# Kernel tuning notes

Measured on AMD Instinct MI355X. Metric: run time of the kernel, lower is better.

## Reference

```python
import jax, jax.numpy as jnp
import numpy as np

N_NODES = 102400   # 256 graphs x 400 nodes
N_EDGES = 1638400  # avg degree 16
C_IN = 128
C_OUT = 128
N_SAGE = 3         # gnn_num
G = 256            # num graphs
M = 400            # nodes per graph (equal-sized -> to_dense_batch is a reshape)


def setup_inputs() -> dict:
    key = jax.random.key(0)
    ks = jax.random.split(key, 6)
    x = jax.random.normal(ks[0], (N_NODES, C_IN), dtype=jnp.float32)
    edge_index = jax.random.randint(ks[1], (2, N_EDGES), 0, N_NODES, dtype=jnp.int32)
    # nodes sorted by graph id, equal graph sizes (matches to_dense_batch assumptions)
    batch = (jnp.arange(N_NODES, dtype=jnp.int32) // M)
    s_in = 1.0 / np.sqrt(C_IN)
    s_out = 1.0 / np.sqrt(C_OUT)
    W_g = jax.random.normal(ks[2], (C_IN, C_OUT), dtype=jnp.float32) * s_in
    b_g = jnp.zeros((C_OUT,), dtype=jnp.float32)
    W_l = jax.random.normal(ks[3], (N_SAGE, C_OUT, C_OUT), dtype=jnp.float32) * s_out  # neighbor lin
    b_l = jnp.zeros((N_SAGE, C_OUT), dtype=jnp.float32)
    W_r = jax.random.normal(ks[4], (N_SAGE, C_OUT, C_OUT), dtype=jnp.float32) * s_out  # root lin (no bias in PyG)
    return {"x": x, "W_g": W_g, "b_g": b_g, "W_l": W_l, "b_l": b_l,
            "W_r": W_r, "edge_index": edge_index, "batch": batch}


def _gcn_conv(x, W, b, src, dst):
    # PyG GCNConv: h = x W; add self loops; norm = d^{-1/2}_src * d^{-1/2}_dst,
    # deg = in-degree at dst counting the self loop; aggregate at dst; add bias.
    h = x @ W                                                     # [N, C_out]
    ones = jnp.ones((N_EDGES,), dtype=h.dtype)
    deg = jax.ops.segment_sum(ones, dst, num_segments=N_NODES) + 1.0
    dinv = jax.lax.rsqrt(deg)                                     # [N]
    norm = dinv[src] * dinv[dst]                                  # [E]
    agg = jax.ops.segment_sum(h[src] * norm[:, None], dst, num_segments=N_NODES)
    agg = agg + h * (dinv * dinv)[:, None]                        # self-loop term
    return agg + b


def _sage_conv(x, W_l, b_l, W_r, src, dst):
    # PyG SAGEConv (mean aggr): out = mean_{j in N(i)} x_j @ W_l + b_l + x @ W_r
    ones = jnp.ones((N_EDGES,), dtype=x.dtype)
    cnt = jax.ops.segment_sum(ones, dst, num_segments=N_NODES)
    s = jax.ops.segment_sum(x[src], dst, num_segments=N_NODES)
    mean = s / jnp.maximum(cnt, 1.0)[:, None]
    return mean @ W_l + b_l + x @ W_r


def _to_dense(x):
    # equal-sized graphs with nodes sorted by batch -> to_dense_batch == reshape
    return x.reshape(G, M, C_OUT)


def reference(x, W_g, b_g, W_l, b_l, W_r, edge_index, batch):
    src, dst = edge_index[0], edge_index[1]
    x = jax.nn.relu(_gcn_conv(x, W_g, b_g, src, dst))
    outs = [_to_dense(x)]
    for i in range(N_SAGE):
        x = jax.nn.relu(_sage_conv(x, W_l[i], b_l[i], W_r[i], src, dst))
        outs.append(_to_dense(x))
    return jnp.stack(outs)  # [N_SAGE+1, G, M, C_OUT]
```

## Files before the change

kernel.cpp:

```cpp
#include <hip/hip_runtime.h>

#define C 128
#define SLOT 64
typedef __attribute__((ext_vector_type(8))) short bf16x8;
typedef __attribute__((ext_vector_type(4))) float f32x4;

__device__ __forceinline__ unsigned short f2bf_rtn(float f) {
    unsigned u = __float_as_uint(f);
    return (unsigned short)((u + 0x7fff + ((u >> 16) & 1)) >> 16);
}
__device__ __forceinline__ float bflo(unsigned u) { return __uint_as_float(u << 16); }
__device__ __forceinline__ float bfhi(unsigned u) { return __uint_as_float(u & 0xffff0000u); }

__device__ __forceinline__ void gload_lds16(const unsigned short* g, unsigned short* l) {
    __builtin_amdgcn_global_load_lds(
        (const __attribute__((address_space(1))) void*)g,
        (__attribute__((address_space(3))) void*)l, 16, 0, 0);
}


__global__ void deg_rank_kernel(const int* __restrict__ ei, int* __restrict__ deg,
                                int* __restrict__ rank, int E) {
    int e = blockIdx.x * blockDim.x + threadIdx.x;
    if (e < E) rank[e] = atomicAdd(&deg[ei[E + e]], 1);
}

__global__ void prep_kernel(const int* __restrict__ deg, float* __restrict__ dinv,
                            float* __restrict__ cinv, int n) {
    int i = blockIdx.x * blockDim.x + threadIdx.x;
    if (i < n) {
        int d = deg[i];
        dinv[i] = rsqrtf((float)(d + 1));
        cinv[i] = 1.0f / (float)max(d, 1);
    }
}


__device__ __forceinline__ void split_bf16(float w, unsigned short& hb, unsigned short& lb) {
    unsigned u = __float_as_uint(w);
    hb = (unsigned short)(u >> 16);
    float hf = __uint_as_float(u & 0xffff0000u);
    lb = (unsigned short)(__float_as_uint(w - hf) >> 16);
}

__global__ __launch_bounds__(256) void wprep_gcn(const float* __restrict__ Wg,
                                                 unsigned short* __restrict__ dst) {
    int idx = blockIdx.x * 256 + threadIdx.x;
    if (idx >= 2 * 128 * 64) return;
    int k64 = idx & 63, ch = (idx >> 6) & 127, chunk = idx >> 13;
    int k = chunk * 64 + k64;
    unsigned short hb, lb;
    split_bf16(Wg[(size_t)k * 128 + ch], hb, lb);
    int pos = (((k64 >> 3) ^ (ch & 7)) << 3) | (k64 & 7);
    size_t base = ((size_t)chunk * 2) * 8192 + ch * 64 + pos;
    dst[base] = hb;
    dst[base + 8192] = lb;
}

__global__ __launch_bounds__(256) void wprep_fused(const float* __restrict__ Wl,
        const float* __restrict__ Wr, unsigned short* __restrict__ dst) {
    int idx = blockIdx.x * 256 + threadIdx.x;
    if (idx >= 3 * 4 * 128 * 64) return;
    int k64 = idx & 63, ch = (idx >> 6) & 127, chunk = (idx >> 13) & 3, layer = idx >> 15;
    int k = chunk * 64 + k64;
    float w = (k < 128) ? Wl[((size_t)layer * 128 + k) * 128 + ch]
                        : Wr[((size_t)layer * 128 + (k - 128)) * 128 + ch];
    unsigned short hb, lb;
    split_bf16(w, hb, lb);
    int pos = (((k64 >> 3) ^ (ch & 7)) << 3) | (k64 & 7);
    size_t base = (((size_t)layer * 4 + chunk) * 2) * 8192 + ch * 64 + pos;
    dst[base] = hb;
    dst[base + 8192] = lb;
}

__global__ __launch_bounds__(256) void csr_gemm_kernel(
        const int* __restrict__ ei, const int* __restrict__ rank,
        int* __restrict__ csr, int E,
        const float* __restrict__ x, const unsigned short* __restrict__ Wp,
        const float* __restrict__ dinv, unsigned short* __restrict__ outbf) {
    __shared__ unsigned short Bs[2][128][64];
    const int b2 = blockIdx.x >> 1;
    const int t = threadIdx.x;

    if (!(blockIdx.x & 1)) {
        const int base = b2 * 1024 + t * 4;
        int4 s4 = *(const int4*)(ei + base);
        int4 d4 = *(const int4*)(ei + E + base);
        int4 r4 = *(const int4*)(rank + base);
        if (r4.x < SLOT) csr[(d4.x << 6) + r4.x] = s4.x;
        if (r4.y < SLOT) csr[(d4.y << 6) + r4.y] = s4.y;
        if (r4.z < SLOT) csr[(d4.z << 6) + r4.z] = s4.z;
        if (r4.w < SLOT) csr[(d4.w << 6) + r4.w] = s4.w;
        return;
    }

    unsigned short* BsFlat = &Bs[0][0][0];
    const int lane = t & 63;
    const int wv = t >> 6;
    const int rowbase = b2 * 64 + wv * 16;
    const int arow = rowbase + (lane & 15);
    const int kq = lane >> 4;

    f32x4 acc[8];
#pragma unroll
    for (int f = 0; f < 8; f++) acc[f] = (f32x4){0.f, 0.f, 0.f, 0.f};

#pragma unroll
    for (int c = 0; c < 2; c++) {
        __syncthreads();
        {
            const unsigned short* srcW = Wp + (size_t)c * 16384;
#pragma unroll
            for (int i = 0; i < 8; i++)
                gload_lds16(srcW + (wv * 8 + i) * 512 + lane * 8,
                            BsFlat + (wv * 8 + i) * 512);
        }
        bf16x8 Ah[2], Al[2];
#pragma unroll
        for (int j = 0; j < 2; j++) {
            const float* base = x + (size_t)arow * C + c * 64 + j * 32;
            float4 x0 = ((const float4*)base)[kq * 2];
            float4 x1 = ((const float4*)base)[kq * 2 + 1];
            float xv[8] = {x0.x, x0.y, x0.z, x0.w, x1.x, x1.y, x1.z, x1.w};
#pragma unroll
            for (int q = 0; q < 8; q++) {
                unsigned u = __float_as_uint(xv[q]);
                Ah[j][q] = (short)(u >> 16);
                float hf = __uint_as_float(u & 0xffff0000u);
                Al[j][q] = (short)(__float_as_uint(xv[q] - hf) >> 16);
            }
        }
        __syncthreads();
#pragma unroll
        for (int j = 0; j < 2; j++) {
#pragma unroll
            for (int f = 0; f < 8; f++) {
                const int chh = f * 16 + (lane & 15);
                const int uu = (j * 4 + kq) ^ (lane & 7);
                bf16x8 bh = *(const bf16x8*)&Bs[0][chh][uu * 8];
                bf16x8 bl = *(const bf16x8*)&Bs[1][chh][uu * 8];
                acc[f] = __builtin_amdgcn_mfma_f32_16x16x32_bf16(Ah[j], bh, acc[f], 0, 0, 0);
                acc[f] = __builtin_amdgcn_mfma_f32_16x16x32_bf16(Al[j], bh, acc[f], 0, 0, 0);
                acc[f] = __builtin_amdgcn_mfma_f32_16x16x32_bf16(Ah[j], bl, acc[f], 0, 0, 0);
            }
        }
    }
    const int col = lane & 15;
    const int rq = lane >> 4;
    float sc[4];
#pragma unroll
    for (int j = 0; j < 4; j++) sc[j] = dinv[rowbase + rq * 4 + j];
#pragma unroll
    for (int f = 0; f < 8; f++)
#pragma unroll
        for (int j = 0; j < 4; j++) {
            const size_t o = (size_t)(rowbase + rq * 4 + j) * C + f * 16 + col;
            outbf[o] = f2bf_rtn(acc[f][j] * sc[j]);
        }
}

template<int WBF>
__global__ __launch_bounds__(256) void gemm_sage(
        const unsigned short* __restrict__ Xbf, const unsigned short* __restrict__ Mbf,
        const unsigned short* __restrict__ Wp, const float* __restrict__ bias,
        float* __restrict__ outf, unsigned short* __restrict__ outbf) {
    __shared__ unsigned short Bs[2][128][64];
    unsigned short* BsFlat = &Bs[0][0][0];
    const int t = threadIdx.x;
    const int lane = t & 63;
    const int wv = t >> 6;
    const int rowbase = blockIdx.x * 64 + wv * 16;
    const int arow = rowbase + (lane & 15);
    const int kq = lane >> 4;

    f32x4 acc[8];
#pragma unroll
    for (int f = 0; f < 8; f++) acc[f] = (f32x4){0.f, 0.f, 0.f, 0.f};

#pragma unroll
    for (int c = 0; c < 4; c++) {
        __syncthreads();
        {
            const unsigned short* srcW = Wp + (size_t)c * 16384;
#pragma unroll
            for (int i = 0; i < 8; i++)
                gload_lds16(srcW + (wv * 8 + i) * 512 + lane * 8,
                            BsFlat + (wv * 8 + i) * 512);
        }
        const unsigned short* tab = (c < 2) ? Mbf : Xbf;
        bf16x8 Ah[2];
#pragma unroll
        for (int j = 0; j < 2; j++)
            Ah[j] = *(const bf16x8*)(tab + (size_t)arow * C + (c & 1) * 64 + j * 32 + kq * 8);
        __syncthreads();
#pragma unroll
        for (int j = 0; j < 2; j++) {
#pragma unroll
            for (int f = 0; f < 8; f++) {
                const int chh = f * 16 + (lane & 15);
                const int uu = (j * 4 + kq) ^ (lane & 7);
                bf16x8 bh = *(const bf16x8*)&Bs[0][chh][uu * 8];
                bf16x8 bl = *(const bf16x8*)&Bs[1][chh][uu * 8];
                acc[f] = __builtin_amdgcn_mfma_f32_16x16x32_bf16(Ah[j], bh, acc[f], 0, 0, 0);
                acc[f] = __builtin_amdgcn_mfma_f32_16x16x32_bf16(Ah[j], bl, acc[f], 0, 0, 0);
            }
        }
    }
    const int col = lane & 15;
    const int rq = lane >> 4;
#pragma unroll
    for (int f = 0; f < 8; f++) {
        const float b = bias[f * 16 + col];
#pragma unroll
        for (int j = 0; j < 4; j++) {
            const size_t o = (size_t)(rowbase + rq * 4 + j) * C + f * 16 + col;
            float v = fmaxf(acc[f][j] + b, 0.f);
            outf[o] = v;
            if (WBF) outbf[o] = f2bf_rtn(v);
        }
    }
}

template<int SELF, int BIASRELU, int WF, int WBF>
__global__ __launch_bounds__(256) void agg_kernel(
        const unsigned short* __restrict__ tbl, const int* __restrict__ csr,
        const int* __restrict__ deg, const float* __restrict__ scale,
        const float* __restrict__ bias, float* __restrict__ outf,
        unsigned short* __restrict__ outbf, int n) {
    const int lane = threadIdx.x & 63;
    const int half = lane >> 5, li = lane & 31;
    const int i = blockIdx.x * 8 + (threadIdx.x >> 6) * 2 + half;
    if (i >= n) return;
    const int dcount = min(deg[i], SLOT);
    const int b = i << 6;
    const int c4 = li * 4;
    float a0 = 0.f, a1 = 0.f, a2 = 0.f, a3 = 0.f;
    for (int base = 0; base < dcount; base += 32) {
        const int cnt = min(32, dcount - base);
        int idx = (base + li < dcount) ? csr[b + base + li] : 0;
        int p = 0;
        for (; p + 4 <= cnt; p += 4) {
            int s0 = __shfl(idx, half * 32 + p);
            int s1 = __shfl(idx, half * 32 + p + 1);
            int s2 = __shfl(idx, half * 32 + p + 2);
            int s3 = __shfl(idx, half * 32 + p + 3);
            uint2 v0 = *(const uint2*)(tbl + (size_t)s0 * C + c4);
            uint2 v1 = *(const uint2*)(tbl + (size_t)s1 * C + c4);
            uint2 v2 = *(const uint2*)(tbl + (size_t)s2 * C + c4);
            uint2 v3 = *(const uint2*)(tbl + (size_t)s3 * C + c4);
            a0 += bflo(v0.x) + bflo(v1.x) + bflo(v2.x) + bflo(v3.x);
            a1 += bfhi(v0.x) + bfhi(v1.x) + bfhi(v2.x) + bfhi(v3.x);
            a2 += bflo(v0.y) + bflo(v1.y) + bflo(v2.y) + bflo(v3.y);
            a3 += bfhi(v0.y) + bfhi(v1.y) + bfhi(v2.y) + bfhi(v3.y);
        }
        for (; p < cnt; p++) {
            int s = __shfl(idx, half * 32 + p);
            uint2 v = *(const uint2*)(tbl + (size_t)s * C + c4);
            a0 += bflo(v.x); a1 += bfhi(v.x);
            a2 += bflo(v.y); a3 += bfhi(v.y);
        }
    }
    if (SELF) {
        uint2 h = *(const uint2*)(tbl + (size_t)i * C + c4);
        a0 += bflo(h.x); a1 += bfhi(h.x);
        a2 += bflo(h.y); a3 += bfhi(h.y);
    }
    const float sc = scale[i];
    a0 *= sc; a1 *= sc; a2 *= sc; a3 *= sc;
    if (BIASRELU) {
        float4 bb = *(const float4*)(bias + c4);
        a0 = fmaxf(a0 + bb.x, 0.f);
        a1 = fmaxf(a1 + bb.y, 0.f);
        a2 = fmaxf(a2 + bb.z, 0.f);
        a3 = fmaxf(a3 + bb.w, 0.f);
    }
    if (WF) {
        float4 r; r.x = a0; r.y = a1; r.z = a2; r.w = a3;
        *(float4*)(outf + (size_t)i * C + c4) = r;
    }
    if (WBF) {
        uint2 pk;
        pk.x = (unsigned)f2bf_rtn(a0) | ((unsigned)f2bf_rtn(a1) << 16);
        pk.y = (unsigned)f2bf_rtn(a2) | ((unsigned)f2bf_rtn(a3) << 16);
        *(uint2*)(outbf + (size_t)i * C + c4) = pk;
    }
}


extern "C" void kernel_launch(void* const* d_in, const int* in_sizes, int n_in,
                              void* d_out, int out_size, void* d_ws, size_t ws_size,
                              hipStream_t stream) {
    const float* x   = (const float*)d_in[0];
    const float* W_g = (const float*)d_in[1];
    const float* b_g = (const float*)d_in[2];
    const float* W_l = (const float*)d_in[3];
    const float* b_l = (const float*)d_in[4];
    const float* W_r = (const float*)d_in[5];
    const int*   ei  = (const int*)d_in[6];

    const int N = in_sizes[0] / C;
    const int E = in_sizes[6] / 2;
    const size_t NC = (size_t)N * C;

    char* ws = (char*)d_ws;
    unsigned short* meanbf = (unsigned short*)ws;
    int* rank = (int*)meanbf;
    unsigned short* tblA   = meanbf + NC;
    unsigned short* tblB   = tblA + NC;
    int* deg  = (int*)(tblB + NC);
    float* dinv = (float*)(deg + N);
    float* cinv = dinv + N;
    unsigned short* wsWg = (unsigned short*)(cinv + N);
    unsigned short* wsWf = wsWg + 32768;

    float* out0 = (float*)d_out;
    int* csr = (int*)(out0 + 3 * NC);

    hipMemsetAsync(deg, 0, (size_t)N * 4, stream);
    deg_rank_kernel<<<(E + 255) / 256, 256, 0, stream>>>(ei, deg, rank, E);
    prep_kernel<<<(N + 255) / 256, 256, 0, stream>>>(deg, dinv, cinv, N);
    wprep_gcn<<<64, 256, 0, stream>>>(W_g, wsWg);
    wprep_fused<<<384, 256, 0, stream>>>(W_l, W_r, wsWf);

    csr_gemm_kernel<<<2 * (N / 64), 256, 0, stream>>>(ei, rank, csr, E,
                                                      x, wsWg, dinv, tblA);

    agg_kernel<1, 1, 1, 1><<<(N + 7) / 8, 256, 0, stream>>>(tblA, csr, deg, dinv,
                                                            b_g, out0, tblB, N);

    const unsigned short* tin[3] = {tblB, tblA, tblB};
    unsigned short* tout[3] = {tblA, tblB, nullptr};
    for (int l = 0; l < 3; l++) {
        float* yout = out0 + (size_t)(l + 1) * NC;
        agg_kernel<0, 0, 0, 1><<<(N + 7) / 8, 256, 0, stream>>>(
            tin[l], csr, deg, cinv, nullptr, nullptr, meanbf, N);
        if (l < 2)
            gemm_sage<1><<<N / 64, 256, 0, stream>>>(tin[l], meanbf,
                wsWf + (size_t)l * 65536, b_l + (size_t)l * C, yout, tout[l]);
        else
            gemm_sage<0><<<N / 64, 256, 0, stream>>>(tin[l], meanbf,
                wsWf + (size_t)l * 65536, b_l + (size_t)l * C, yout, nullptr);
    }
}
```

Measured before the change: 456.1 us.

## Fuse degree counting into GEMM launch and merge setup kernels

```diff
diff --git a/kernel.cpp b/kernel.cpp
--- a/kernel.cpp
+++ b/kernel.cpp
@@ -17,24 +17,6 @@
         (const __attribute__((address_space(1))) void*)g,
         (__attribute__((address_space(3))) void*)l, 16, 0, 0);
 }
-
-
-__global__ void deg_rank_kernel(const int* __restrict__ ei, int* __restrict__ deg,
-                                int* __restrict__ rank, int E) {
-    int e = blockIdx.x * blockDim.x + threadIdx.x;
-    if (e < E) rank[e] = atomicAdd(&deg[ei[E + e]], 1);
-}
-
-__global__ void prep_kernel(const int* __restrict__ deg, float* __restrict__ dinv,
-                            float* __restrict__ cinv, int n) {
-    int i = blockIdx.x * blockDim.x + threadIdx.x;
-    if (i < n) {
-        int d = deg[i];
-        dinv[i] = rsqrtf((float)(d + 1));
-        cinv[i] = 1.0f / (float)max(d, 1);
-    }
-}
-
 
 __device__ __forceinline__ void split_bf16(float w, unsigned short& hb, unsigned short& lb) {
     unsigned u = __float_as_uint(w);
@@ -43,23 +25,22 @@
     lb = (unsigned short)(__float_as_uint(w - hf) >> 16);
 }
 
-__global__ __launch_bounds__(256) void wprep_gcn(const float* __restrict__ Wg,
-                                                 unsigned short* __restrict__ dst) {
+__global__ __launch_bounds__(256) void wprep_all(const float* __restrict__ Wg,
+        const float* __restrict__ Wl, const float* __restrict__ Wr,
+        unsigned short* __restrict__ dstG, unsigned short* __restrict__ dstF) {
     int idx = blockIdx.x * 256 + threadIdx.x;
-    if (idx >= 2 * 128 * 64) return;
-    int k64 = idx & 63, ch = (idx >> 6) & 127, chunk = idx >> 13;
-    int k = chunk * 64 + k64;
-    unsigned short hb, lb;
-    split_bf16(Wg[(size_t)k * 128 + ch], hb, lb);
-    int pos = (((k64 >> 3) ^ (ch & 7)) << 3) | (k64 & 7);
-    size_t base = ((size_t)chunk * 2) * 8192 + ch * 64 + pos;
-    dst[base] = hb;
-    dst[base + 8192] = lb;
-}
-
-__global__ __launch_bounds__(256) void wprep_fused(const float* __restrict__ Wl,
-        const float* __restrict__ Wr, unsigned short* __restrict__ dst) {
-    int idx = blockIdx.x * 256 + threadIdx.x;
+    if (idx < 16384) {
+        int k64 = idx & 63, ch = (idx >> 6) & 127, chunk = idx >> 13;
+        int k = chunk * 64 + k64;
+        unsigned short hb, lb;
+        split_bf16(Wg[(size_t)k * 128 + ch], hb, lb);
+        int pos = (((k64 >> 3) ^ (ch & 7)) << 3) | (k64 & 7);
+        size_t base = ((size_t)chunk * 2) * 8192 + ch * 64 + pos;
+        dstG[base] = hb;
+        dstG[base + 8192] = lb;
+        return;
+    }
+    idx -= 16384;
     if (idx >= 3 * 4 * 128 * 64) return;
     int k64 = idx & 63, ch = (idx >> 6) & 127, chunk = (idx >> 13) & 3, layer = idx >> 15;
     int k = chunk * 64 + k64;
@@ -69,28 +50,27 @@
     split_bf16(w, hb, lb);
     int pos = (((k64 >> 3) ^ (ch & 7)) << 3) | (k64 & 7);
     size_t base = (((size_t)layer * 4 + chunk) * 2) * 8192 + ch * 64 + pos;
-    dst[base] = hb;
-    dst[base + 8192] = lb;
-}
-
-__global__ __launch_bounds__(256) void csr_gemm_kernel(
-        const int* __restrict__ ei, const int* __restrict__ rank,
-        int* __restrict__ csr, int E,
+    dstF[base] = hb;
+    dstF[base + 8192] = lb;
+}
+
+__global__ __launch_bounds__(256) void build_gemm_kernel(
+        const int* __restrict__ ei, int* __restrict__ deg, int* __restrict__ rank, int E,
         const float* __restrict__ x, const unsigned short* __restrict__ Wp,
-        const float* __restrict__ dinv, unsigned short* __restrict__ outbf) {
+        unsigned short* __restrict__ outbf) {
     __shared__ unsigned short Bs[2][128][64];
     const int b2 = blockIdx.x >> 1;
     const int t = threadIdx.x;
 
     if (!(blockIdx.x & 1)) {
         const int base = b2 * 1024 + t * 4;
-        int4 s4 = *(const int4*)(ei + base);
         int4 d4 = *(const int4*)(ei + E + base);
-        int4 r4 = *(const int4*)(rank + base);
-        if (r4.x < SLOT) csr[(d4.x << 6) + r4.x] = s4.x;
-        if (r4.y < SLOT) csr[(d4.y << 6) + r4.y] = s4.y;
-        if (r4.z < SLOT) csr[(d4.z << 6) + r4.z] = s4.z;
-        if (r4.w < SLOT) csr[(d4.w << 6) + r4.w] = s4.w;
+        int4 r;
+        r.x = atomicAdd(&deg[d4.x], 1);
+        r.y = atomicAdd(&deg[d4.y], 1);
+        r.z = atomicAdd(&deg[d4.z], 1);
+        r.w = atomicAdd(&deg[d4.w], 1);
+        *(int4*)(rank + base) = r;
         return;
     }
 
@@ -147,16 +127,50 @@
     }
     const int col = lane & 15;
     const int rq = lane >> 4;
-    float sc[4];
-#pragma unroll
-    for (int j = 0; j < 4; j++) sc[j] = dinv[rowbase + rq * 4 + j];
 #pragma unroll
     for (int f = 0; f < 8; f++)
 #pragma unroll
         for (int j = 0; j < 4; j++) {
             const size_t o = (size_t)(rowbase + rq * 4 + j) * C + f * 16 + col;
-            outbf[o] = f2bf_rtn(acc[f][j] * sc[j]);
-        }
+            outbf[o] = f2bf_rtn(acc[f][j]);
+        }
+}
+
+__global__ __launch_bounds__(256) void scatter_scale_kernel(
+        const int* __restrict__ ei, const int* __restrict__ rank,
+        int* __restrict__ csr, int E, const int* __restrict__ deg,
+        unsigned short* __restrict__ tbl, float* __restrict__ dinv,
+        float* __restrict__ cinv, int n) {
+    const int SB = E >> 10;
+    const int t = threadIdx.x;
+    if (blockIdx.x < SB) {
+        const int base = blockIdx.x * 1024 + t * 4;
+        int4 s4 = *(const int4*)(ei + base);
+        int4 d4 = *(const int4*)(ei + E + base);
+        int4 r4 = *(const int4*)(rank + base);
+        if (r4.x < SLOT) csr[(d4.x << 6) + r4.x] = s4.x;
+        if (r4.y < SLOT) csr[(d4.y << 6) + r4.y] = s4.y;
+        if (r4.z < SLOT) csr[(d4.z << 6) + r4.z] = s4.z;
+        if (r4.w < SLOT) csr[(d4.w << 6) + r4.w] = s4.w;
+        return;
+    }
+    const int rb = (blockIdx.x - SB) * 16 + (t >> 4);
+    if (rb >= n) return;
+    const int ch = (t & 15) * 8;
+    const int d = deg[rb];
+    const float di = rsqrtf((float)(d + 1));
+    if ((t & 15) == 0) {
+        dinv[rb] = di;
+        cinv[rb] = 1.0f / (float)max(d, 1);
+    }
+    unsigned short* row = tbl + (size_t)rb * C + ch;
+    uint4 v = *(const uint4*)row;
+    uint4 w;
+    w.x = (unsigned)f2bf_rtn(bflo(v.x) * di) | ((unsigned)f2bf_rtn(bfhi(v.x) * di) << 16);
+    w.y = (unsigned)f2bf_rtn(bflo(v.y) * di) | ((unsigned)f2bf_rtn(bfhi(v.y) * di) << 16);
+    w.z = (unsigned)f2bf_rtn(bflo(v.z) * di) | ((unsigned)f2bf_rtn(bfhi(v.z) * di) << 16);
+    w.w = (unsigned)f2bf_rtn(bflo(v.w) * di) | ((unsigned)f2bf_rtn(bfhi(v.w) * di) << 16);
+    *(uint4*)row = w;
 }
 
 template<int WBF>
@@ -239,6 +253,32 @@
         const int cnt = min(32, dcount - base);
         int idx = (base + li < dcount) ? csr[b + base + li] : 0;
         int p = 0;
+        for (; p + 8 <= cnt; p += 8) {
+            int s0 = __shfl(idx, half * 32 + p);
+            int s1 = __shfl(idx, half * 32 + p + 1);
+            int s2 = __shfl(idx, half * 32 + p + 2);
+            int s3 = __shfl(idx, half * 32 + p + 3);
+            int s4 = __shfl(idx, half * 32 + p + 4);
+            int s5 = __shfl(idx, half * 32 + p + 5);
+            int s6 = __shfl(idx, half * 32 + p + 6);
+            int s7 = __shfl(idx, half * 32 + p + 7);
+            uint2 v0 = *(const uint2*)(tbl + (size_t)s0 * C + c4);
+            uint2 v1 = *(const uint2*)(tbl + (size_t)s1 * C + c4);
+            uint2 v2 = *(const uint2*)(tbl + (size_t)s2 * C + c4);
+            uint2 v3 = *(const uint2*)(tbl + (size_t)s3 * C + c4);
+            uint2 v4 = *(const uint2*)(tbl + (size_t)s4 * C + c4);
+            uint2 v5 = *(const uint2*)(tbl + (size_t)s5 * C + c4);
+            uint2 v6 = *(const uint2*)(tbl + (size_t)s6 * C + c4);
+            uint2 v7 = *(const uint2*)(tbl + (size_t)s7 * C + c4);
+            a0 += bflo(v0.x) + bflo(v1.x) + bflo(v2.x) + bflo(v3.x)
+                + bflo(v4.x) + bflo(v5.x) + bflo(v6.x) + bflo(v7.x);
+            a1 += bfhi(v0.x) + bfhi(v1.x) + bfhi(v2.x) + bfhi(v3.x)
+                + bfhi(v4.x) + bfhi(v5.x) + bfhi(v6.x) + bfhi(v7.x);
+            a2 += bflo(v0.y) + bflo(v1.y) + bflo(v2.y) + bflo(v3.y)
+                + bflo(v4.y) + bflo(v5.y) + bflo(v6.y) + bflo(v7.y);
+            a3 += bfhi(v0.y) + bfhi(v1.y) + bfhi(v2.y) + bfhi(v3.y)
+                + bfhi(v4.y) + bfhi(v5.y) + bfhi(v6.y) + bfhi(v7.y);
+        }
         for (; p + 4 <= cnt; p += 4) {
             int s0 = __shfl(idx, half * 32 + p);
             int s1 = __shfl(idx, half * 32 + p + 1);
@@ -317,13 +357,12 @@
     int* csr = (int*)(out0 + 3 * NC);
 
     hipMemsetAsync(deg, 0, (size_t)N * 4, stream);
-    deg_rank_kernel<<<(E + 255) / 256, 256, 0, stream>>>(ei, deg, rank, E);
-    prep_kernel<<<(N + 255) / 256, 256, 0, stream>>>(deg, dinv, cinv, N);
-    wprep_gcn<<<64, 256, 0, stream>>>(W_g, wsWg);
-    wprep_fused<<<384, 256, 0, stream>>>(W_l, W_r, wsWf);
-
-    csr_gemm_kernel<<<2 * (N / 64), 256, 0, stream>>>(ei, rank, csr, E,
-                                                      x, wsWg, dinv, tblA);
+    wprep_all<<<448, 256, 0, stream>>>(W_g, W_l, W_r, wsWg, wsWf);
+
+    build_gemm_kernel<<<2 * (N / 64), 256, 0, stream>>>(ei, deg, rank, E,
+                                                        x, wsWg, tblA);
+    scatter_scale_kernel<<<(E >> 10) + N / 16, 256, 0, stream>>>(
+        ei, rank, csr, E, deg, tblA, dinv, cinv, N);
 
     agg_kernel<1, 1, 1, 1><<<(N + 7) / 8, 256, 0, stream>>>(tblA, csr, deg, dinv,
                                                             b_g, out0, tblB, N);
```

After: 424.5 us. 1.07x faster.
